# Performance work log

Measured on AMD Instinct MI355X. Metric: run time of the kernel, lower is better.

The kernel has to match this reference:

```python
import jax, jax.numpy as jnp
import numpy as np

B, D, IN_F, OUT_F, BLOCK = 2, 1024, 4096, 4096, 128
N_BLOCKS = IN_F // BLOCK  # 32


def setup_inputs() -> dict:
    key = jax.random.key(0)
    k1, k2, k3 = jax.random.split(key, 3)
    inputs = jax.random.normal(k1, (B, D, IN_F), dtype=jnp.float32)
    # int8 quantized weight buffer: [n_blocks, block_size, out_features]
    weight = jax.random.randint(k2, (N_BLOCKS, BLOCK, OUT_F), -128, 128, dtype=jnp.int32).astype(jnp.int8)
    # per-block, per-output-channel scaler: [n_blocks, out_features]
    weight_scaler = (jax.random.uniform(k3, (N_BLOCKS, OUT_F), dtype=jnp.float32) * 0.01 + 0.001)
    return {"inputs": inputs, "weight": weight, "weight_scaler": weight_scaler}


def reference(inputs, weight, weight_scaler):
    # Faithful port of WeightOnlyBlockwiseQuantizedLinear.blockwise_jax_kernel
    # (default path: symmetric quantization, zero_point is None).
    weight = weight.astype(jnp.int8)
    block_size = weight.shape[1]
    b, d, in_f = inputs.shape
    # [b, d, n_blocks s, block_size c]
    x = inputs.reshape(b, d, in_f // block_size, block_size)
    # per-block int8 matmul (promoted to float32 by x): [b, d, s, z]
    out = jnp.einsum("scz,bdsc->bdsz", weight, x)
    # apply per-block scaler and reduce over blocks: [b, d, z]
    out = jnp.einsum("bdsz,sz->bdz", out, weight_scaler)
    return out
```

## Files before the change

kernel.cpp:

```cpp
#include <hip/hip_runtime.h>
#include <hip/hip_bf16.h>


#define MDIM 2048
#define NDIM 4096
#define KDIM 4096
#define NBLK 32
#define BM 128
#define BN 256
#define BK 64
#define NT (KDIM / BK)

typedef __attribute__((ext_vector_type(8))) short bf16x8;
typedef __attribute__((ext_vector_type(4))) float f32x4;
typedef __attribute__((ext_vector_type(8))) unsigned short u16x8;

__device__ __forceinline__ unsigned short f2bf(float f) {
  unsigned u = __float_as_uint(f);
  u += 0x7fffu + ((u >> 16) & 1u);
  return (unsigned short)(u >> 16);
}

__device__ __forceinline__ void gl_lds16(const void* g, void* l) {
  __builtin_amdgcn_global_load_lds(
      (const __attribute__((address_space(1))) unsigned int*)g,
      (__attribute__((address_space(3))) unsigned int*)l,
      16, 0, 0);
}

__global__ void prep_a_kernel(const float* __restrict__ x,
                              unsigned short* __restrict__ ab) {
  int i = blockIdx.x * blockDim.x + threadIdx.x;
  const float4 v = reinterpret_cast<const float4*>(x)[i];
  ushort4 hv;
  hv.x = f2bf(v.x); hv.y = f2bf(v.y); hv.z = f2bf(v.z); hv.w = f2bf(v.w);
  reinterpret_cast<ushort4*>(ab)[i] = hv;
}

__global__ void prep_b_kernel(const int* __restrict__ w,
                              const float* __restrict__ scaler,
                              unsigned short* __restrict__ bt) {
  const int t = threadIdx.x;
  const int n0 = blockIdx.x * 128;
  const int k0 = blockIdx.y * 128;
  const int s = blockIdx.y;
  const int k8 = (t & 15) * 8;
  const int n8 = (t >> 4) * 8;

  float sc[8];
  {
    const float4* scv = reinterpret_cast<const float4*>(scaler + (size_t)s * NDIM + n0 + n8);
    const float4 s0 = scv[0], s1 = scv[1];
    sc[0] = s0.x; sc[1] = s0.y; sc[2] = s0.z; sc[3] = s0.w;
    sc[4] = s1.x; sc[5] = s1.y; sc[6] = s1.z; sc[7] = s1.w;
  }
  u16x8 outv[8];
#pragma unroll
  for (int r = 0; r < 8; ++r) {
    const int4* src = reinterpret_cast<const int4*>(w + (size_t)(k0 + k8 + r) * NDIM + n0 + n8);
    const int4 a = src[0], b = src[1];
    const int v[8] = {a.x, a.y, a.z, a.w, b.x, b.y, b.z, b.w};
#pragma unroll
    for (int j = 0; j < 8; ++j) outv[j][r] = f2bf((float)v[j] * sc[j]);
  }
#pragma unroll
  for (int j = 0; j < 8; ++j)
    *reinterpret_cast<u16x8*>(bt + (size_t)(n0 + n8 + j) * KDIM + k0 + k8) = outv[j];
}

#define MFMA_BF16 __builtin_amdgcn_mfma_f32_16x16x32_bf16

__global__ __launch_bounds__(512, 2)
void gemm_kernel(const unsigned short* __restrict__ ab,
                 const unsigned short* __restrict__ bt,
                 float* __restrict__ out) {
  __shared__ __align__(16) char lds[98304];

  const int t = threadIdx.x;
  const int lane = t & 63;
  const int wid = t >> 6;
  const int wm = wid >> 2;
  const int wn = wid & 3;
  const int lane15 = lane & 15;
  const int laneq = lane >> 4;
  const int swz = (lane & 7) << 4;

  const unsigned flat = blockIdx.x;
  const unsigned swzb = (flat & 7u) * 32u + (flat >> 3);
  const int ntile = swzb & 15;
  const int mtile = swzb >> 4;
  const int m0 = mtile * BM;
  const int n0 = ntile * BN;

  const int srow = t >> 3;
  const int sslot = (t & 7) ^ (srow & 7);
  const char* ga = (const char*)ab + ((size_t)(m0 + srow) * KDIM) * 2 + sslot * 16;
  const char* gb = (const char*)bt + ((size_t)(n0 + srow) * KDIM) * 2 + sslot * 16;
  const size_t rstep = (size_t)64 * KDIM * 2;

  char* const lA0 = lds + (size_t)wid * 1024;
  char* const lB0 = lds + 32768 + (size_t)wid * 1024;

#define STAGE(kt, c) do {                                   \
    const size_t ko_ = (size_t)(kt) * (BK * 2);             \
    char* a_ = lA0 + (c) * 16384;                           \
    char* b_ = lB0 + (c) * 32768;                           \
    gl_lds16(ga + ko_,             a_);                     \
    gl_lds16(ga + ko_ + rstep,     a_ + 8192);              \
    gl_lds16(gb + ko_,             b_);                     \
    gl_lds16(gb + ko_ + rstep,     b_ + 8192);              \
    gl_lds16(gb + ko_ + 2 * rstep, b_ + 16384);             \
    gl_lds16(gb + ko_ + 3 * rstep, b_ + 24576);             \
  } while (0)

  int offA[4], offB[4];
#pragma unroll
  for (int i = 0; i < 4; ++i) {
    offA[i] = (wm * 64 + i * 16 + lane15) * 128 + laneq * 16;
    offB[i] = (wn * 64 + i * 16 + lane15) * 128 + laneq * 16;
  }

  const f32x4 fzero = {0.f, 0.f, 0.f, 0.f};
  f32x4 acc[4][4];
#pragma unroll
  for (int m = 0; m < 4; ++m)
#pragma unroll
    for (int n = 0; n < 4; ++n) acc[m][n] = fzero;

  bf16x8 af[4][2];
  bf16x8 bfr[2][4][2];

#define LDA(m, base) do {                                             \
    af[m][0] = *(const bf16x8*)((base) + ((offA[m]) ^ swz));          \
    af[m][1] = *(const bf16x8*)((base) + ((offA[m] + 64) ^ swz));     \
  } while (0)
#define LDB(S, n, base) do {                                          \
    bfr[S][n][0] = *(const bf16x8*)((base) + ((offB[n]) ^ swz));      \
    bfr[S][n][1] = *(const bf16x8*)((base) + ((offB[n] + 64) ^ swz)); \
  } while (0)
#define HALF(mA, mB, P) do {                                               \
    acc[mA][0] = MFMA_BF16(af[mA][0], bfr[P][0][0], acc[mA][0], 0, 0, 0);  \
    acc[mA][1] = MFMA_BF16(af[mA][0], bfr[P][1][0], acc[mA][1], 0, 0, 0);  \
    acc[mA][2] = MFMA_BF16(af[mA][0], bfr[P][2][0], acc[mA][2], 0, 0, 0);  \
    acc[mA][3] = MFMA_BF16(af[mA][0], bfr[P][3][0], acc[mA][3], 0, 0, 0);  \
    acc[mB][0] = MFMA_BF16(af[mB][0], bfr[P][0][0], acc[mB][0], 0, 0, 0);  \
    acc[mB][1] = MFMA_BF16(af[mB][0], bfr[P][1][0], acc[mB][1], 0, 0, 0);  \
    acc[mB][2] = MFMA_BF16(af[mB][0], bfr[P][2][0], acc[mB][2], 0, 0, 0);  \
    acc[mB][3] = MFMA_BF16(af[mB][0], bfr[P][3][0], acc[mB][3], 0, 0, 0);  \
    acc[mA][0] = MFMA_BF16(af[mA][1], bfr[P][0][1], acc[mA][0], 0, 0, 0);  \
    acc[mA][1] = MFMA_BF16(af[mA][1], bfr[P][1][1], acc[mA][1], 0, 0, 0);  \
    acc[mA][2] = MFMA_BF16(af[mA][1], bfr[P][2][1], acc[mA][2], 0, 0, 0);  \
    acc[mA][3] = MFMA_BF16(af[mA][1], bfr[P][3][1], acc[mA][3], 0, 0, 0);  \
    acc[mB][0] = MFMA_BF16(af[mB][1], bfr[P][0][1], acc[mB][0], 0, 0, 0);  \
    acc[mB][1] = MFMA_BF16(af[mB][1], bfr[P][1][1], acc[mB][1], 0, 0, 0);  \
    acc[mB][2] = MFMA_BF16(af[mB][1], bfr[P][2][1], acc[mB][2], 0, 0, 0);  \
    acc[mB][3] = MFMA_BF16(af[mB][1], bfr[P][3][1], acc[mB][3], 0, 0, 0);  \
  } while (0)

#define BODY(t2, P) do {                                                   \
    char* lac = lds + (P) * 16384;                                         \
                                                        \
    LDA(2, lac); LDA(3, lac);                                              \
    __builtin_amdgcn_s_barrier();                                          \
    __builtin_amdgcn_s_setprio(1);                                         \
    HALF(0, 1, P);                                                         \
    __builtin_amdgcn_s_setprio(0);                                         \
    asm volatile("s_waitcnt lgkmcnt(0)" ::: "memory"); \
    __builtin_amdgcn_s_barrier();                                          \
                                                        \
    if ((t2) + 2 < NT) {                                                   \
      STAGE((t2) + 2, P);                                                  \
      asm volatile("s_waitcnt vmcnt(6)" ::: "memory");    \
    } else {                                                               \
      asm volatile("s_waitcnt vmcnt(0)" ::: "memory");                     \
    }                                                                      \
    __builtin_amdgcn_s_barrier();                                          \
    __builtin_amdgcn_sched_barrier(0);                                     \
    if ((t2) + 1 < NT) {                                                   \
      char* nac = lds + (1 - (P)) * 16384;                                 \
      char* nbc = lds + 32768 + (1 - (P)) * 32768;                         \
      LDA(0, nac); LDA(1, nac);                                            \
      LDB(1 - (P), 0, nbc); LDB(1 - (P), 1, nbc);                          \
      LDB(1 - (P), 2, nbc); LDB(1 - (P), 3, nbc);                          \
    }                                                                      \
    __builtin_amdgcn_s_setprio(1);                                         \
    HALF(2, 3, P);                                                         \
    __builtin_amdgcn_s_setprio(0);                                         \
    __builtin_amdgcn_s_barrier();                                          \
  } while (0)

  STAGE(0, 0);
  STAGE(1, 1);
  asm volatile("s_waitcnt vmcnt(6)" ::: "memory");
  __builtin_amdgcn_s_barrier();
  {
    char* nac = lds;
    char* nbc = lds + 32768;
    LDA(0, nac); LDA(1, nac);
    LDB(0, 0, nbc); LDB(0, 1, nbc); LDB(0, 2, nbc); LDB(0, 3, nbc);
  }

  for (int t2 = 0; t2 < NT; t2 += 2) {
    BODY(t2, 0);
    BODY(t2 + 1, 1);
  }

#pragma unroll
  for (int m = 0; m < 4; ++m)
#pragma unroll
    for (int r = 0; r < 4; ++r) {
      const int row = m0 + wm * 64 + m * 16 + laneq * 4 + r;
      float* op = out + (size_t)row * NDIM + n0 + wn * 64 + lane15;
#pragma unroll
      for (int n = 0; n < 4; ++n) op[n * 16] = acc[m][n][r];
    }
#undef STAGE
#undef LDA
#undef LDB
#undef HALF
#undef BODY
}

__global__ void fallback_kernel(const float* __restrict__ x,
                                const int* __restrict__ w,
                                const float* __restrict__ scaler,
                                float* __restrict__ out) {
  const int n = blockIdx.x * 256 + threadIdx.x;
  const int m = blockIdx.y;
  float acc = 0.f;
  for (int s = 0; s < NBLK; ++s) {
    float p = 0.f;
    const float* xr = x + (size_t)m * KDIM + s * 128;
    const int* wr = w + (size_t)s * 128 * NDIM + n;
#pragma unroll 8
    for (int c = 0; c < 128; ++c) p += xr[c] * (float)wr[(size_t)c * NDIM];
    acc += p * scaler[s * NDIM + n];
  }
  out[(size_t)m * NDIM + n] = acc;
}

extern "C" void kernel_launch(void* const* d_in, const int* in_sizes, int n_in,
                              void* d_out, int out_size, void* d_ws, size_t ws_size,
                              hipStream_t stream) {
  (void)in_sizes; (void)n_in; (void)out_size;
  const float* x = (const float*)d_in[0];
  const int* w = (const int*)d_in[1];
  const float* sc = (const float*)d_in[2];
  float* out = (float*)d_out;

  const size_t need = (size_t)51 * 1024 * 1024;
  if (ws_size >= need) {
    unsigned short* ab = (unsigned short*)d_ws;
    unsigned short* bt = ab + (size_t)MDIM * KDIM;
    prep_a_kernel<<<(MDIM * KDIM / 4) / 256, 256, 0, stream>>>(x, ab);
    prep_b_kernel<<<dim3(NDIM / 128, KDIM / 128), 256, 0, stream>>>(w, sc, bt);
    gemm_kernel<<<(MDIM / BM) * (NDIM / BN), 512, 0, stream>>>(ab, bt, out);
  } else {
    fallback_kernel<<<dim3(NDIM / 256, MDIM), 256, 0, stream>>>(x, w, sc, out);
  }
}
```

Measured before the change: 208.1 us.

## Switch GEMM mainloop to triple-buffered LDS with simplified per-k-step schedule

Replaces the double-buffered LDS pipeline, which used register double-buffering of B fragments and split MFMA halves, with a three-buffer LDS ring. Each k-tile is now issued two tiles ahead. Each k-tile loads A and B fragments for two k-substeps and runs 16 MFMAs per substep, separated by barriers and a full lgkmcnt wait. The goal is to give global loads more time to land and to simplify the schedule. In exchange, LDS use per block rises to 144KB, and LDS fragment reads are no longer overlapped with MFMAs inside a wave.

```diff
diff --git a/kernel.cpp b/kernel.cpp
--- a/kernel.cpp
+++ b/kernel.cpp
@@ -10,6 +10,7 @@
 #define BN 256
 #define BK 64
 #define NT (KDIM / BK)
+#define BUFSZ 49152
 
 typedef __attribute__((ext_vector_type(8))) short bf16x8;
 typedef __attribute__((ext_vector_type(4))) float f32x4;
@@ -74,7 +75,7 @@
 void gemm_kernel(const unsigned short* __restrict__ ab,
                  const unsigned short* __restrict__ bt,
                  float* __restrict__ out) {
-  __shared__ __align__(16) char lds[98304];
+  __shared__ __align__(16) char lds[3 * BUFSZ];
 
   const int t = threadIdx.x;
   const int lane = t & 63;
@@ -98,13 +99,12 @@
   const char* gb = (const char*)bt + ((size_t)(n0 + srow) * KDIM) * 2 + sslot * 16;
   const size_t rstep = (size_t)64 * KDIM * 2;
 
-  char* const lA0 = lds + (size_t)wid * 1024;
-  char* const lB0 = lds + 32768 + (size_t)wid * 1024;
-
-#define STAGE(kt, c) do {                                   \
+  const int ldwave = wid * 1024;
+
+#define STAGE(kt, buf) do {                                 \
     const size_t ko_ = (size_t)(kt) * (BK * 2);             \
-    char* a_ = lA0 + (c) * 16384;                           \
-    char* b_ = lB0 + (c) * 32768;                           \
+    char* a_ = lds + (buf) * BUFSZ + ldwave;                \
+    char* b_ = lds + (buf) * BUFSZ + 16384 + ldwave;        \
     gl_lds16(ga + ko_,             a_);                     \
     gl_lds16(ga + ko_ + rstep,     a_ + 8192);              \
     gl_lds16(gb + ko_,             b_);                     \
@@ -127,82 +127,77 @@
 #pragma unroll
     for (int n = 0; n < 4; ++n) acc[m][n] = fzero;
 
-  bf16x8 af[4][2];
-  bf16x8 bfr[2][4][2];
-
-#define LDA(m, base) do {                                             \
-    af[m][0] = *(const bf16x8*)((base) + ((offA[m]) ^ swz));          \
-    af[m][1] = *(const bf16x8*)((base) + ((offA[m] + 64) ^ swz));     \
+#define LD8(KS, la_, lb_) do {                                        \
+    f[0] = *(const bf16x8*)((la_) + ((offA[0] + (KS) * 64) ^ swz));   \
+    f[1] = *(const bf16x8*)((la_) + ((offA[1] + (KS) * 64) ^ swz));   \
+    f[2] = *(const bf16x8*)((la_) + ((offA[2] + (KS) * 64) ^ swz));   \
+    f[3] = *(const bf16x8*)((la_) + ((offA[3] + (KS) * 64) ^ swz));   \
+    g[0] = *(const bf16x8*)((lb_) + ((offB[0] + (KS) * 64) ^ swz));   \
+    g[1] = *(const bf16x8*)((lb_) + ((offB[1] + (KS) * 64) ^ swz));   \
+    g[2] = *(const bf16x8*)((lb_) + ((offB[2] + (KS) * 64) ^ swz));   \
+    g[3] = *(const bf16x8*)((lb_) + ((offB[3] + (KS) * 64) ^ swz));   \
   } while (0)
-#define LDB(S, n, base) do {                                          \
-    bfr[S][n][0] = *(const bf16x8*)((base) + ((offB[n]) ^ swz));      \
-    bfr[S][n][1] = *(const bf16x8*)((base) + ((offB[n] + 64) ^ swz)); \
-  } while (0)
-#define HALF(mA, mB, P) do {                                               \
-    acc[mA][0] = MFMA_BF16(af[mA][0], bfr[P][0][0], acc[mA][0], 0, 0, 0);  \
-    acc[mA][1] = MFMA_BF16(af[mA][0], bfr[P][1][0], acc[mA][1], 0, 0, 0);  \
-    acc[mA][2] = MFMA_BF16(af[mA][0], bfr[P][2][0], acc[mA][2], 0, 0, 0);  \
-    acc[mA][3] = MFMA_BF16(af[mA][0], bfr[P][3][0], acc[mA][3], 0, 0, 0);  \
-    acc[mB][0] = MFMA_BF16(af[mB][0], bfr[P][0][0], acc[mB][0], 0, 0, 0);  \
-    acc[mB][1] = MFMA_BF16(af[mB][0], bfr[P][1][0], acc[mB][1], 0, 0, 0);  \
-    acc[mB][2] = MFMA_BF16(af[mB][0], bfr[P][2][0], acc[mB][2], 0, 0, 0);  \
-    acc[mB][3] = MFMA_BF16(af[mB][0], bfr[P][3][0], acc[mB][3], 0, 0, 0);  \
-    acc[mA][0] = MFMA_BF16(af[mA][1], bfr[P][0][1], acc[mA][0], 0, 0, 0);  \
-    acc[mA][1] = MFMA_BF16(af[mA][1], bfr[P][1][1], acc[mA][1], 0, 0, 0);  \
-    acc[mA][2] = MFMA_BF16(af[mA][1], bfr[P][2][1], acc[mA][2], 0, 0, 0);  \
-    acc[mA][3] = MFMA_BF16(af[mA][1], bfr[P][3][1], acc[mA][3], 0, 0, 0);  \
-    acc[mB][0] = MFMA_BF16(af[mB][1], bfr[P][0][1], acc[mB][0], 0, 0, 0);  \
-    acc[mB][1] = MFMA_BF16(af[mB][1], bfr[P][1][1], acc[mB][1], 0, 0, 0);  \
-    acc[mB][2] = MFMA_BF16(af[mB][1], bfr[P][2][1], acc[mB][2], 0, 0, 0);  \
-    acc[mB][3] = MFMA_BF16(af[mB][1], bfr[P][3][1], acc[mB][3], 0, 0, 0);  \
-  } while (0)
-
-#define BODY(t2, P) do {                                                   \
-    char* lac = lds + (P) * 16384;                                         \
-                                                        \
-    LDA(2, lac); LDA(3, lac);                                              \
-    __builtin_amdgcn_s_barrier();                                          \
-    __builtin_amdgcn_s_setprio(1);                                         \
-    HALF(0, 1, P);                                                         \
-    __builtin_amdgcn_s_setprio(0);                                         \
-    asm volatile("s_waitcnt lgkmcnt(0)" ::: "memory"); \
-    __builtin_amdgcn_s_barrier();                                          \
-                                                        \
-    if ((t2) + 2 < NT) {                                                   \
-      STAGE((t2) + 2, P);                                                  \
-      asm volatile("s_waitcnt vmcnt(6)" ::: "memory");    \
-    } else {                                                               \
-      asm volatile("s_waitcnt vmcnt(0)" ::: "memory");                     \
-    }                                                                      \
-    __builtin_amdgcn_s_barrier();                                          \
-    __builtin_amdgcn_sched_barrier(0);                                     \
-    if ((t2) + 1 < NT) {                                                   \
-      char* nac = lds + (1 - (P)) * 16384;                                 \
-      char* nbc = lds + 32768 + (1 - (P)) * 32768;                         \
-      LDA(0, nac); LDA(1, nac);                                            \
-      LDB(1 - (P), 0, nbc); LDB(1 - (P), 1, nbc);                          \
-      LDB(1 - (P), 2, nbc); LDB(1 - (P), 3, nbc);                          \
-    }                                                                      \
-    __builtin_amdgcn_s_setprio(1);                                         \
-    HALF(2, 3, P);                                                         \
-    __builtin_amdgcn_s_setprio(0);                                         \
-    __builtin_amdgcn_s_barrier();                                          \
+
+#define MF16() do {                                          \
+    acc[0][0] = MFMA_BF16(f[0], g[0], acc[0][0], 0, 0, 0);   \
+    acc[0][1] = MFMA_BF16(f[0], g[1], acc[0][1], 0, 0, 0);   \
+    acc[0][2] = MFMA_BF16(f[0], g[2], acc[0][2], 0, 0, 0);   \
+    acc[0][3] = MFMA_BF16(f[0], g[3], acc[0][3], 0, 0, 0);   \
+    acc[1][0] = MFMA_BF16(f[1], g[0], acc[1][0], 0, 0, 0);   \
+    acc[1][1] = MFMA_BF16(f[1], g[1], acc[1][1], 0, 0, 0);   \
+    acc[1][2] = MFMA_BF16(f[1], g[2], acc[1][2], 0, 0, 0);   \
+    acc[1][3] = MFMA_BF16(f[1], g[3], acc[1][3], 0, 0, 0);   \
+    acc[2][0] = MFMA_BF16(f[2], g[0], acc[2][0], 0, 0, 0);   \
+    acc[2][1] = MFMA_BF16(f[2], g[1], acc[2][1], 0, 0, 0);   \
+    acc[2][2] = MFMA_BF16(f[2], g[2], acc[2][2], 0, 0, 0);   \
+    acc[2][3] = MFMA_BF16(f[2], g[3], acc[2][3], 0, 0, 0);   \
+    acc[3][0] = MFMA_BF16(f[3], g[0], acc[3][0], 0, 0, 0);   \
+    acc[3][1] = MFMA_BF16(f[3], g[1], acc[3][1], 0, 0, 0);   \
+    acc[3][2] = MFMA_BF16(f[3], g[2], acc[3][2], 0, 0, 0);   \
+    acc[3][3] = MFMA_BF16(f[3], g[3], acc[3][3], 0, 0, 0);   \
   } while (0)
 
   STAGE(0, 0);
   STAGE(1, 1);
   asm volatile("s_waitcnt vmcnt(6)" ::: "memory");
   __builtin_amdgcn_s_barrier();
-  {
-    char* nac = lds;
-    char* nbc = lds + 32768;
-    LDA(0, nac); LDA(1, nac);
-    LDB(0, 0, nbc); LDB(0, 1, nbc); LDB(0, 2, nbc); LDB(0, 3, nbc);
-  }
-
-  for (int t2 = 0; t2 < NT; t2 += 2) {
-    BODY(t2, 0);
-    BODY(t2 + 1, 1);
+
+  int c = 0, cn = 2;
+  for (int kt = 0; kt < NT; ++kt) {
+    const char* la_ = lds + c * BUFSZ;
+    const char* lb_ = la_ + 16384;
+    bf16x8 f[4], g[4];
+
+    LD8(0, la_, lb_);
+    if (kt + 2 < NT) STAGE(kt + 2, cn);
+    __builtin_amdgcn_sched_barrier(0);
+    __builtin_amdgcn_s_barrier();
+    asm volatile("s_waitcnt lgkmcnt(0)" ::: "memory");
+    __builtin_amdgcn_sched_barrier(0);
+    __builtin_amdgcn_s_setprio(1);
+    MF16();
+    __builtin_amdgcn_s_setprio(0);
+    __builtin_amdgcn_sched_barrier(0);
+    __builtin_amdgcn_s_barrier();
+
+    LD8(1, la_, lb_);
+    __builtin_amdgcn_sched_barrier(0);
+    __builtin_amdgcn_s_barrier();
+    asm volatile("s_waitcnt lgkmcnt(0)" ::: "memory");
+    __builtin_amdgcn_sched_barrier(0);
+    __builtin_amdgcn_s_setprio(1);
+    MF16();
+    __builtin_amdgcn_s_setprio(0);
+    __builtin_amdgcn_sched_barrier(0);
+    if (kt + 2 < NT) {
+      asm volatile("s_waitcnt vmcnt(6)" ::: "memory");
+    } else {
+      asm volatile("s_waitcnt vmcnt(0)" ::: "memory");
+    }
+    __builtin_amdgcn_s_barrier();
+
+    c = (c == 2) ? 0 : c + 1;
+    cn = (cn == 2) ? 0 : cn + 1;
   }
 
 #pragma unroll
@@ -215,10 +210,8 @@
       for (int n = 0; n < 4; ++n) op[n * 16] = acc[m][n][r];
     }
 #undef STAGE
-#undef LDA
-#undef LDB
-#undef HALF
-#undef BODY
+#undef LD8
+#undef MF16
 }
 
 __global__ void fallback_kernel(const float* __restrict__ x,
```

Result: slower. 215.2 us (+3.4%).
